# Kernel optimization log

Measured on AMD Instinct MI355X. Metric: run time of the kernel, lower is better.

The kernel has to match this reference:

```python
import jax, jax.numpy as jnp
import numpy as np

HID = 10     # hidden_size
IN = 4       # input_size
OUT = 4
P = 5        # predict_ahead


def setup_inputs() -> dict:
    key = jax.random.key(0)
    ks = jax.random.split(key, 7)
    B, T = 16384, 100
    x = jax.random.normal(ks[0], (B, T, IN), dtype=jnp.float32)
    s = 1.0 / np.sqrt(HID)  # PyTorch default uniform init bound
    W_ih = jax.random.uniform(ks[1], (4 * HID, IN), jnp.float32, -s, s)
    W_hh = jax.random.uniform(ks[2], (4 * HID, HID), jnp.float32, -s, s)
    b_ih = jax.random.uniform(ks[3], (4 * HID,), jnp.float32, -s, s)
    b_hh = jax.random.uniform(ks[4], (4 * HID,), jnp.float32, -s, s)
    W_lin = jax.random.uniform(ks[5], (OUT, HID), jnp.float32, -s, s)
    b_lin = jax.random.uniform(ks[6], (OUT,), jnp.float32, -s, s)
    return {"x": x, "W_ih": W_ih, "W_hh": W_hh, "b_ih": b_ih,
            "b_hh": b_hh, "W_lin": W_lin, "b_lin": b_lin}


def _lstm_cell(xt, h, c, W_ih, W_hh, b_ih, b_hh):
    # PyTorch gate order: i, f, g, o
    gates = xt @ W_ih.T + h @ W_hh.T + (b_ih + b_hh)  # [B, 4H]
    i, f, g, o = jnp.split(gates, 4, axis=-1)
    c_new = jax.nn.sigmoid(f) * c + jax.nn.sigmoid(i) * jnp.tanh(g)
    h_new = jax.nn.sigmoid(o) * jnp.tanh(c_new)
    return h_new, c_new


def reference(x, W_ih, W_hh, b_ih, b_hh, W_lin, b_lin):
    B, T, _ = x.shape
    Tp = T - P + 1  # number of outer time steps
    h0 = jnp.zeros((B, HID), x.dtype)
    c0 = jnp.zeros((B, HID), x.dtype)
    xs = jnp.transpose(x[:, :Tp, :], (1, 0, 2))  # [Tp, B, IN]

    def step(carry, xt):
        h, c = carry
        h, c = _lstm_cell(xt, h, c, W_ih, W_hh, b_ih, b_hh)
        y = h @ W_lin.T + b_lin  # [B, OUT]
        outs = [y]
        h_a, c_a = h, c
        for _ in range(P - 1):
            h_a, c_a = _lstm_cell(y, h_a, c_a, W_ih, W_hh, b_ih, b_hh)
            y = h_a @ W_lin.T + b_lin
            outs.append(y)
        return (h, c), jnp.stack(outs, axis=1)  # [B, P, OUT]

    (h, c), ys = jax.lax.scan(step, (h0, c0), xs)  # ys: [Tp, B, P, OUT]
    final_output = jnp.transpose(ys, (1, 0, 2, 3))  # [B, Tp, P, OUT]
    return final_output, c[None]  # c_t: [num_layers=1, B, HID]
```

## Files before the change

### kernel.cpp

```cpp
#include <hip/hip_runtime.h>


#define HIDN 10
#define INPN 4
#define OUTN 4
#define PN   5
#define TN   100
#define TPN  96
#define BN   16384
#define GPB  24

typedef float v2f __attribute__((ext_vector_type(2)));

#define PIN(x) asm volatile("" : "+v"(x))

__device__ __forceinline__ float rcpf_(float v) { return __builtin_amdgcn_rcpf(v); }
__device__ __forceinline__ float e2_(float v)   { return __builtin_amdgcn_exp2f(v); }
__device__ __forceinline__ float sig2_(float g)  { return rcpf_(1.0f + e2_(-g)); }
__device__ __forceinline__ float tanh2_(float g) { return fmaf(-2.0f, rcpf_(1.0f + e2_(g)), 1.0f); }

#define K2L2E 2.88539008177792681472f

__global__ __launch_bounds__(256, 2) void lstm_ar_kernel(
    const float* __restrict__ x,
    const float* __restrict__ W_ih,
    const float* __restrict__ W_hh,
    const float* __restrict__ b_ih,
    const float* __restrict__ b_hh,
    const float* __restrict__ W_lin,
    const float* __restrict__ b_lin,
    float* __restrict__ out)
{
    __shared__ __align__(16) float s_h[GPB][6][20];

    const int tid = threadIdx.x;
    const int wid = tid >> 6;
    const int wl  = tid & 63;
    const int grp = wl / 10;
    const int u   = wl - grp * 10;
    const int slot  = wid * 6 + grp;
    const int batch = blockIdx.x * GPB + slot;
    if (grp >= 6 || batch >= BN) return;

    const float L2E = 1.44269504088896340736f;
    const float rs[4] = { L2E, L2E, 2.0f * L2E, L2E };

    v2f  wm2[4][5];
    v2f  wc2[4][5];
    v2f  wih2[4][2];
    v2f  bm2[4];
    v2f  br2[4];
    #pragma unroll
    for (int r = 0; r < 4; ++r) {
        const int j = u + r * 10;
        float wihr[INPN];
        #pragma unroll
        for (int q = 0; q < INPN; ++q) wihr[q] = W_ih[j * INPN + q];
        float bmr = b_ih[j] + b_hh[j];
        float brr = bmr;
        #pragma unroll
        for (int q = 0; q < INPN; ++q) brr += wihr[q] * b_lin[q];
        #pragma unroll
        for (int k = 0; k < HIDN; ++k) {
            float wmk = W_hh[j * HIDN + k];
            float wck = wmk;
            #pragma unroll
            for (int q = 0; q < INPN; ++q) wck += wihr[q] * W_lin[q * HIDN + k];
            if (k & 1) { wm2[r][k >> 1].y = wmk * rs[r]; wc2[r][k >> 1].y = wck * rs[r]; }
            else       { wm2[r][k >> 1].x = wmk * rs[r]; wc2[r][k >> 1].x = wck * rs[r]; }
        }
        #pragma unroll
        for (int q = 0; q < INPN; ++q) {
            if (q & 1) wih2[r][q >> 1].y = wihr[q] * rs[r];
            else       wih2[r][q >> 1].x = wihr[q] * rs[r];
        }
        bm2[r] = v2f{ bmr * rs[r], 0.0f };
        br2[r] = v2f{ brr * rs[r], 0.0f };
    }

    const int pmine = u >> 1;
    const int opair = (u & 1) * 2;
    v2f yl0[5], yl1[5];
    #pragma unroll
    for (int k = 0; k < HIDN; k += 2) {
        yl0[k >> 1] = v2f{ W_lin[opair * HIDN + k],       W_lin[opair * HIDN + k + 1] };
        yl1[k >> 1] = v2f{ W_lin[(opair + 1) * HIDN + k], W_lin[(opair + 1) * HIDN + k + 1] };
    }
    v2f ybv0 = v2f{ b_lin[opair],     0.0f };
    v2f ybv1 = v2f{ b_lin[opair + 1], 0.0f };

    #pragma unroll
    for (int r = 0; r < 4; ++r) {
        #pragma unroll
        for (int k = 0; k < 5; ++k) { PIN(wm2[r][k]); PIN(wc2[r][k]); }
        PIN(wih2[r][0]); PIN(wih2[r][1]); PIN(bm2[r]); PIN(br2[r]);
    }
    #pragma unroll
    for (int k = 0; k < 5; ++k) { PIN(yl0[k]); PIN(yl1[k]); }
    PIN(ybv0); PIN(ybv1);

    const float* xb   = x + (long)batch * TN * INPN;
    float*       outb = out + (long)batch * TPN * PN * OUTN;

    float cm = 0.0f;
    v2f h2m[5], h2n[5];
    #pragma unroll
    for (int k = 0; k < 5; ++k) h2m[k] = v2f{0.0f, 0.0f};

    auto CELL = [&](const float g[4], float& c) -> float {
        float iv = sig2_(g[0]), fv = sig2_(g[1]), gv = tanh2_(g[2]), ov = sig2_(g[3]);
        c = fmaf(fv, c, iv * gv);
        return ov * tanh2_(c * K2L2E);
    };

    auto MAIN = [&](int t, float4 xv) {
        v2f xa = v2f{xv.x, xv.y}, xc = v2f{xv.z, xv.w};
        float g[4];
        #pragma unroll
        for (int r = 0; r < 4; ++r) {
            v2f acc = bm2[r];
            acc = __builtin_elementwise_fma(wih2[r][0], xa, acc);
            acc = __builtin_elementwise_fma(wih2[r][1], xc, acc);
            #pragma unroll
            for (int k = 0; k < 5; ++k)
                acc = __builtin_elementwise_fma(wm2[r][k], h2m[k], acc);
            g[r] = acc.x + acc.y;
        }
        float hn = CELL(g, cm);
        s_h[slot][t & 1][u] = hn;
        __builtin_amdgcn_wave_barrier();
        const v2f* hp = (const v2f*)&s_h[slot][t & 1][0];
        #pragma unroll
        for (int k = 0; k < 5; ++k) h2n[k] = hp[k];
    };

    auto ROLLOUT = [&](int tt, float cro) {
        v2f hr2[5];
        #pragma unroll
        for (int k = 0; k < 5; ++k) hr2[k] = h2m[k];
        float cr = cro;
        float g[4];
        #pragma unroll
        for (int p = 1; p < PN; ++p) {
            #pragma unroll
            for (int r = 0; r < 4; ++r) {
                v2f acc = br2[r];
                #pragma unroll
                for (int k = 0; k < 5; ++k)
                    acc = __builtin_elementwise_fma(wc2[r][k], hr2[k], acc);
                g[r] = acc.x + acc.y;
            }
            float hn = CELL(g, cr);
            s_h[slot][1 + p][u] = hn;
            __builtin_amdgcn_wave_barrier();
            if (p < PN - 1) {
                const v2f* hp = (const v2f*)&s_h[slot][1 + p][0];
                #pragma unroll
                for (int k = 0; k < 5; ++k) hr2[k] = hp[k];
            }
        }
        const int rowy = (pmine == 0) ? (tt & 1) : (pmine + 1);
        const v2f* hq = (const v2f*)&s_h[slot][rowy][0];
        v2f h0 = hq[0], h1 = hq[1], h3 = hq[2], h4 = hq[3], h5 = hq[4];
        v2f a0 = ybv0, a1 = ybv1;
        a0 = __builtin_elementwise_fma(yl0[0], h0, a0);
        a1 = __builtin_elementwise_fma(yl1[0], h0, a1);
        a0 = __builtin_elementwise_fma(yl0[1], h1, a0);
        a1 = __builtin_elementwise_fma(yl1[1], h1, a1);
        a0 = __builtin_elementwise_fma(yl0[2], h3, a0);
        a1 = __builtin_elementwise_fma(yl1[2], h3, a1);
        a0 = __builtin_elementwise_fma(yl0[3], h4, a0);
        a1 = __builtin_elementwise_fma(yl1[3], h4, a1);
        a0 = __builtin_elementwise_fma(yl0[4], h5, a0);
        a1 = __builtin_elementwise_fma(yl1[4], h5, a1);
        float2 yv; yv.x = a0.x + a0.y; yv.y = a1.x + a1.y;
        *(float2*)(outb + tt * PN * OUTN + 2 * u) = yv;
    };

    float4 xcur = *(const float4*)xb;
    MAIN(0, xcur);
    xcur = *(const float4*)(xb + INPN);

    for (int t = 1; t < TPN; ++t) {
        float4 xnext = *(const float4*)(xb + (t + 1) * INPN);
        #pragma unroll
        for (int k = 0; k < 5; ++k) h2m[k] = h2n[k];
        float cro = cm;
        MAIN(t, xcur);
        ROLLOUT(t - 1, cro);
        xcur = xnext;
    }

    #pragma unroll
    for (int k = 0; k < 5; ++k) h2m[k] = h2n[k];
    ROLLOUT(TPN - 1, cm);

    out[(long)BN * TPN * PN * OUTN + (long)batch * HIDN + u] = cm;
}

extern "C" void kernel_launch(void* const* d_in, const int* in_sizes, int n_in,
                              void* d_out, int out_size, void* d_ws, size_t ws_size,
                              hipStream_t stream) {
    const float* x     = (const float*)d_in[0];
    const float* W_ih  = (const float*)d_in[1];
    const float* W_hh  = (const float*)d_in[2];
    const float* b_ih  = (const float*)d_in[3];
    const float* b_hh  = (const float*)d_in[4];
    const float* W_lin = (const float*)d_in[5];
    const float* b_lin = (const float*)d_in[6];
    float* out = (float*)d_out;

    const int grid = (BN + GPB - 1) / GPB;
    lstm_ar_kernel<<<grid, 256, 0, stream>>>(x, W_ih, W_hh, b_ih, b_hh, W_lin, b_lin, out);
}
```

Before: 192.2 us.

## Reuse composed rollout weights in main step via y-correction to cut registers

Drops the separate W_hh weight and bias registers for the main LSTM step. The main step now reuses the composed rollout weights (W_hh + W_ih·W_lin) and feeds in the input difference x - y_prev. y_prev is computed per step by two lanes and shared through LDS. The lower register use allows raising launch bounds from 2 to 3 waves per SIMD. The cost is an extra small matvec, an LDS round trip and a wave barrier on the serial critical path, plus possible rounding differences from the algebraic rewrite.

```diff
diff --git a/kernel.cpp b/kernel.cpp
--- a/kernel.cpp
+++ b/kernel.cpp
@@ -21,7 +21,7 @@
 
 #define K2L2E 2.88539008177792681472f
 
-__global__ __launch_bounds__(256, 2) void lstm_ar_kernel(
+__global__ __launch_bounds__(256, 3) void lstm_ar_kernel(
     const float* __restrict__ x,
     const float* __restrict__ W_ih,
     const float* __restrict__ W_hh,
@@ -32,6 +32,7 @@
     float* __restrict__ out)
 {
     __shared__ __align__(16) float s_h[GPB][6][20];
+    __shared__ __align__(16) float s_y[GPB][4];
 
     const int tid = threadIdx.x;
     const int wid = tid >> 6;
@@ -45,10 +46,8 @@
     const float L2E = 1.44269504088896340736f;
     const float rs[4] = { L2E, L2E, 2.0f * L2E, L2E };
 
-    v2f  wm2[4][5];
     v2f  wc2[4][5];
     v2f  wih2[4][2];
-    v2f  bm2[4];
     v2f  br2[4];
     #pragma unroll
     for (int r = 0; r < 4; ++r) {
@@ -56,25 +55,22 @@
         float wihr[INPN];
         #pragma unroll
         for (int q = 0; q < INPN; ++q) wihr[q] = W_ih[j * INPN + q];
-        float bmr = b_ih[j] + b_hh[j];
-        float brr = bmr;
+        float brr = b_ih[j] + b_hh[j];
         #pragma unroll
         for (int q = 0; q < INPN; ++q) brr += wihr[q] * b_lin[q];
         #pragma unroll
         for (int k = 0; k < HIDN; ++k) {
-            float wmk = W_hh[j * HIDN + k];
-            float wck = wmk;
+            float wck = W_hh[j * HIDN + k];
             #pragma unroll
             for (int q = 0; q < INPN; ++q) wck += wihr[q] * W_lin[q * HIDN + k];
-            if (k & 1) { wm2[r][k >> 1].y = wmk * rs[r]; wc2[r][k >> 1].y = wck * rs[r]; }
-            else       { wm2[r][k >> 1].x = wmk * rs[r]; wc2[r][k >> 1].x = wck * rs[r]; }
+            if (k & 1) wc2[r][k >> 1].y = wck * rs[r];
+            else       wc2[r][k >> 1].x = wck * rs[r];
         }
         #pragma unroll
         for (int q = 0; q < INPN; ++q) {
             if (q & 1) wih2[r][q >> 1].y = wihr[q] * rs[r];
             else       wih2[r][q >> 1].x = wihr[q] * rs[r];
         }
-        bm2[r] = v2f{ bmr * rs[r], 0.0f };
         br2[r] = v2f{ brr * rs[r], 0.0f };
     }
 
@@ -92,8 +88,8 @@
     #pragma unroll
     for (int r = 0; r < 4; ++r) {
         #pragma unroll
-        for (int k = 0; k < 5; ++k) { PIN(wm2[r][k]); PIN(wc2[r][k]); }
-        PIN(wih2[r][0]); PIN(wih2[r][1]); PIN(bm2[r]); PIN(br2[r]);
+        for (int k = 0; k < 5; ++k) PIN(wc2[r][k]);
+        PIN(wih2[r][0]); PIN(wih2[r][1]); PIN(br2[r]);
     }
     #pragma unroll
     for (int k = 0; k < 5; ++k) { PIN(yl0[k]); PIN(yl1[k]); }
@@ -113,17 +109,33 @@
         return ov * tanh2_(c * K2L2E);
     };
 
+    auto SY = [&]() {
+        if (u < 2) {
+            v2f a0 = ybv0, a1 = ybv1;
+            #pragma unroll
+            for (int k = 0; k < 5; ++k) {
+                a0 = __builtin_elementwise_fma(yl0[k], h2m[k], a0);
+                a1 = __builtin_elementwise_fma(yl1[k], h2m[k], a1);
+            }
+            float2 yv; yv.x = a0.x + a0.y; yv.y = a1.x + a1.y;
+            *(float2*)&s_y[slot][2 * u] = yv;
+        }
+        __builtin_amdgcn_wave_barrier();
+    };
+
     auto MAIN = [&](int t, float4 xv) {
-        v2f xa = v2f{xv.x, xv.y}, xc = v2f{xv.z, xv.w};
+        float4 yp = *(const float4*)&s_y[slot][0];
+        v2f dxa = v2f{xv.x - yp.x, xv.y - yp.y};
+        v2f dxc = v2f{xv.z - yp.z, xv.w - yp.w};
         float g[4];
         #pragma unroll
         for (int r = 0; r < 4; ++r) {
-            v2f acc = bm2[r];
-            acc = __builtin_elementwise_fma(wih2[r][0], xa, acc);
-            acc = __builtin_elementwise_fma(wih2[r][1], xc, acc);
+            v2f acc = br2[r];
+            acc = __builtin_elementwise_fma(wih2[r][0], dxa, acc);
+            acc = __builtin_elementwise_fma(wih2[r][1], dxc, acc);
             #pragma unroll
             for (int k = 0; k < 5; ++k)
-                acc = __builtin_elementwise_fma(wm2[r][k], h2m[k], acc);
+                acc = __builtin_elementwise_fma(wc2[r][k], h2m[k], acc);
             g[r] = acc.x + acc.y;
         }
         float hn = CELL(g, cm);
@@ -178,6 +190,7 @@
     };
 
     float4 xcur = *(const float4*)xb;
+    SY();
     MAIN(0, xcur);
     xcur = *(const float4*)(xb + INPN);
 
@@ -186,6 +199,7 @@
         #pragma unroll
         for (int k = 0; k < 5; ++k) h2m[k] = h2n[k];
         float cro = cm;
+        SY();
         MAIN(t, xcur);
         ROLLOUT(t - 1, cro);
         xcur = xnext;
```

New measurement: 191.6 us. Within noise of the previous version (-0.3%).
